# Kernel tuning notes

Measured on AMD Instinct MI355X. Metric: run time of the kernel, lower is better.

The kernel has to match this reference:

```python
import jax, jax.numpy as jnp
import numpy as np

N = 100_000   # nodes
E = 1_600_000 # edges
D = 128       # hidden/input dim
OUT = 32      # output dim
G = 512       # graphs in batch
L = 3         # conv layers


def setup_inputs() -> dict:
    key = jax.random.key(0)
    ks = jax.random.split(key, 12)
    s = 1.0 / np.sqrt(D)
    inp = {
        "x": jax.random.normal(ks[0], (N, D), jnp.float32),
        "edge_index": jax.random.randint(ks[1], (2, E), 0, N, dtype=jnp.int32),
        "batch": jnp.sort(jax.random.randint(ks[2], (N,), 0, G, dtype=jnp.int32)),
        "enc_W1": jax.random.normal(ks[3], (D, D), jnp.float32) * s,
        "enc_b1": jnp.zeros((D,), jnp.float32),
        "enc_W2": jax.random.normal(ks[4], (D, D), jnp.float32) * s,
        "enc_b2": jnp.zeros((D,), jnp.float32),
        "gcn_W": jax.random.normal(ks[5], (L, D, D), jnp.float32) * s,
        "gcn_b": jnp.zeros((L, D), jnp.float32),
        "dec_W1": jax.random.normal(ks[6], (D, D), jnp.float32) * s,
        "dec_b1": jnp.zeros((D,), jnp.float32),
        "dec_W2": jax.random.normal(ks[7], (D, OUT), jnp.float32) * s,
        "dec_b2": jnp.zeros((OUT,), jnp.float32),
        "num_graphs": G,
    }
    return inp


def reference(x, edge_index, batch, enc_W1, enc_b1, enc_W2, enc_b2,
              gcn_W, gcn_b, dec_W1, dec_b1, dec_W2, dec_b2, num_graphs):
    n = x.shape[0]
    src, dst = edge_index[0], edge_index[1]

    # ---- encoder MLP (Linear -> ReLU -> Linear -> ReLU) ----
    h = jax.nn.relu(x @ enc_W1 + enc_b1)
    h = jax.nn.relu(h @ enc_W2 + enc_b2)

    # ---- GCN normalization: D^{-1/2} (A + I) D^{-1/2}, degrees incl. self-loops ----
    deg = jax.ops.segment_sum(jnp.ones_like(src, dtype=h.dtype), dst, num_segments=n) + 1.0
    inv_sqrt = jax.lax.rsqrt(deg)           # [N]
    edge_coef = inv_sqrt[src] * inv_sqrt[dst]  # [E]
    self_coef = inv_sqrt * inv_sqrt            # [N]

    # ---- GCN conv layers ----
    for l in range(gcn_W.shape[0]):
        hw = h @ gcn_W[l]                                       # [N, D]
        msgs = hw[src] * edge_coef[:, None]                     # [E, D] gather
        agg = jax.ops.segment_sum(msgs, dst, num_segments=n)    # [N, D] scatter-add
        agg = agg + hw * self_coef[:, None]                     # self loops
        h = jax.nn.relu(agg + gcn_b[l])

    # ---- global add pool over graphs ----
    pooled = jax.ops.segment_sum(h, batch, num_segments=num_graphs)  # [G, D]

    # ---- decoder MLP ----
    out = jax.nn.relu(pooled @ dec_W1 + dec_b1)
    return out @ dec_W2 + dec_b2
```

## Files before the change

kernel.cpp:

```cpp
#include <hip/hip_runtime.h>

#define NNODES 100000
#define NEDGES 1600000
#define DIM    128
#define OUTD   32
#define NGRAPH 512

#define NBUCK2  256
#define BSHIFT  9
#define CAP     12288
#define EPB2    8192
#define SBLOCKS ((NEDGES + EPB2 - 1) / EPB2)
#define NBUILD  ((NNODES + 511) / 512)
#define EBLOCKS ((NNODES + 63) / 64)
#define AGGBLK  ((NNODES + 31) / 32)

using bf16x8 = __attribute__((ext_vector_type(8))) short;
using f32x4  = __attribute__((ext_vector_type(4))) float;
using f32x2  = __attribute__((ext_vector_type(2))) float;

__device__ __forceinline__ short f2bf(float f) {
    unsigned u = __float_as_uint(f);
    unsigned r = (u + 0x7fff + ((u >> 16) & 1)) >> 16;
    return (short)r;
}
__device__ __forceinline__ float bf2f(short s) {
    return __uint_as_float(((unsigned)(unsigned short)s) << 16);
}

__device__ __forceinline__ uint2 bf8_to_fp8(bf16x8 t) {
    float f0 = bf2f(t[0]), f1 = bf2f(t[1]), f2 = bf2f(t[2]), f3 = bf2f(t[3]);
    float f4 = bf2f(t[4]), f5 = bf2f(t[5]), f6 = bf2f(t[6]), f7 = bf2f(t[7]);
    uint2 o;
    o.x = __builtin_amdgcn_cvt_pk_fp8_f32(f0, f1, 0, false);
    o.x = __builtin_amdgcn_cvt_pk_fp8_f32(f2, f3, o.x, true);
    o.y = __builtin_amdgcn_cvt_pk_fp8_f32(f4, f5, 0, false);
    o.y = __builtin_amdgcn_cvt_pk_fp8_f32(f6, f7, o.y, true);
    return o;
}

__global__ __launch_bounds__(256) void k_prep(
    const float* __restrict__ eW1, const float* __restrict__ eW2,
    const float* __restrict__ gW, short* __restrict__ WT,
    int* __restrict__ gcur, float* __restrict__ pooled)
{
    int idx = blockIdx.x * 256 + threadIdx.x;
    if (idx < 5 * 16384) {
        int mat = idx >> 14, rem = idx & 16383;
        int k = rem >> 7, n = rem & 127;
        const float* src = (mat == 0) ? eW1 : (mat == 1) ? eW2
                                            : (gW + (size_t)(mat - 2) * 16384);
        WT[(size_t)mat * 16384 + n * DIM + k] = f2bf(src[k * DIM + n]);
    }
    if (idx < NBUCK2) gcur[idx] = idx * CAP;
    if (idx < NGRAPH * DIM) pooled[idx] = 0.f;
}

__global__ __launch_bounds__(512) void k_scatter(
    const int* __restrict__ src, const int* __restrict__ dst,
    int* __restrict__ gcur, unsigned* __restrict__ tmp)
{
    __shared__ unsigned short rnk[EPB2];
    __shared__ int h[NBUCK2];
    __shared__ int gbase[NBUCK2];
    const int tid  = threadIdx.x;
    const int base = blockIdx.x * EPB2;
    if (tid < NBUCK2) h[tid] = 0;
    __syncthreads();
    #pragma unroll
    for (int it = 0; it < EPB2 / 512; ++it) {
        int e = base + it * 512 + tid;
        if (e < NEDGES) {
            int b = dst[e] >> BSHIFT;
            rnk[it * 512 + tid] = (unsigned short)atomicAdd(&h[b], 1);
        }
    }
    __syncthreads();
    if (tid < NBUCK2 && h[tid] > 0)
        gbase[tid] = atomicAdd(&gcur[tid], h[tid]);
    __syncthreads();
    #pragma unroll
    for (int it = 0; it < EPB2 / 512; ++it) {
        int e = base + it * 512 + tid;
        if (e < NEDGES) {
            int d = dst[e], sv = src[e];
            int b = d >> BSHIFT;
            int pos = gbase[b] + rnk[it * 512 + tid];
            if (pos < (b + 1) * CAP)
                tmp[pos] = (unsigned)sv | ((unsigned)(d & 511) << 17);
        }
    }
}

__global__ __launch_bounds__(512) void k_build(
    const unsigned* __restrict__ tmp, const int* __restrict__ gcur,
    int* __restrict__ row_off, int* __restrict__ cntA,
    float* __restrict__ inv, int* __restrict__ col)
{
    __shared__ int hist[512], sc[512], lcur[512];
    const int tid   = threadIdx.x;
    const int b     = blockIdx.x;
    const int tbase = b * CAP;
    const int cnt_b = min(gcur[b] - tbase, CAP);
    hist[tid] = 0;
    __syncthreads();
    for (int i = tid; i < cnt_b; i += 512)
        atomicAdd(&hist[(tmp[tbase + i] >> 17) & 511], 1);
    __syncthreads();
    const int hv = hist[tid];
    sc[tid] = hv;
    __syncthreads();
    for (int off = 1; off < 512; off <<= 1) {
        int t = (tid >= off) ? sc[tid - off] : 0;
        __syncthreads();
        sc[tid] += t;
        __syncthreads();
    }
    const int start = tbase + sc[tid] - hv;
    lcur[tid] = start;
    const int node = b * 512 + tid;
    if (node < NNODES) {
        row_off[node] = start;
        cntA[node]    = hv;
        inv[node]     = rsqrtf((float)hv + 1.0f);
    }
    __syncthreads();
    for (int i = tid; i < cnt_b; i += 512) {
        unsigned t = tmp[tbase + i];
        int pos = atomicAdd(&lcur[(t >> 17) & 511], 1);
        col[pos] = (int)((t & 0x1FFFFu) << 7);
    }
}

__global__ __launch_bounds__(512, 6) void k_enc(
    const float* __restrict__ x, const short* __restrict__ WT,
    const float* __restrict__ b1, const float* __restrict__ b2,
    const float* __restrict__ inv, unsigned char* __restrict__ g8, int M)
{
    __shared__ short As[64 * 128];
    __shared__ short Bs[128 * 128];

    const int tid = threadIdx.x;
    const int m0  = blockIdx.x * 64;

    #pragma unroll
    for (int i = 0; i < 2; ++i) {
        int u = tid + i * 512;
        int row = u >> 4, c = u & 15;
        int gr = min(m0 + row, M - 1);
        const float4* sp = (const float4*)(x + (size_t)gr * DIM + (c << 3));
        float4 f0 = sp[0], f1 = sp[1];
        short t8[8] = { f2bf(f0.x), f2bf(f0.y), f2bf(f0.z), f2bf(f0.w),
                        f2bf(f1.x), f2bf(f1.y), f2bf(f1.z), f2bf(f1.w) };
        *(bf16x8*)&As[row * 128 + ((c ^ (row & 15)) << 3)] = *(bf16x8*)t8;
    }

    const int wave = tid >> 6, lane = tid & 63;
    const int ml = lane & 15, quad = lane >> 4;
    const int rw = wave >> 1;
    const int cw = wave & 1;

    #pragma unroll
    for (int mat = 0; mat < 3; ++mat) {
        if (mat > 0) __syncthreads();
        #pragma unroll
        for (int i = 0; i < 4; ++i) {
            int u = tid + i * 512;
            int n = u >> 4, c = u & 15;
            *(bf16x8*)&Bs[n * 128 + ((c ^ (n & 15)) << 3)] =
                *(const bf16x8*)(WT + (size_t)mat * 16384 + n * DIM + (c << 3));
        }
        __syncthreads();

        f32x4 acc[4] = {};
        const int arow = rw * 16 + ml;
        #pragma unroll
        for (int kk = 0; kk < 4; ++kk) {
            const int c = kk * 4 + quad;
            bf16x8 a = *(bf16x8*)&As[arow * 128 + ((c ^ (arow & 15)) << 3)];
            #pragma unroll
            for (int ni = 0; ni < 4; ++ni) {
                const int brow = (cw * 4 + ni) * 16 + ml;
                bf16x8 b = *(bf16x8*)&Bs[brow * 128 + ((c ^ (brow & 15)) << 3)];
                acc[ni] = __builtin_amdgcn_mfma_f32_16x16x32_bf16(a, b, acc[ni], 0, 0, 0);
            }
        }
        __syncthreads();

        #pragma unroll
        for (int ni = 0; ni < 4; ++ni) {
            const int colc = cw * 64 + ni * 16 + ml;
            const int cc = colc >> 3, w = colc & 7;
            #pragma unroll
            for (int r = 0; r < 4; ++r) {
                const int rowl = rw * 16 + quad * 4 + r;
                float v = acc[ni][r];
                if (mat == 0)      v = fmaxf(v + b1[colc], 0.f);
                else if (mat == 1) v = fmaxf(v + b2[colc], 0.f);
                else               v *= inv[min(m0 + rowl, M - 1)];
                As[rowl * 128 + (((cc ^ (rowl & 15)) << 3) | w)] = f2bf(v);
            }
        }
    }
    __syncthreads();

    #pragma unroll
    for (int i = 0; i < 2; ++i) {
        int u = tid + i * 512;
        int row = u >> 4, c = u & 15;
        int gr = m0 + row;
        if (gr < M) {
            bf16x8 t = *(bf16x8*)&As[row * 128 + ((c ^ (row & 15)) << 3)];
            *(uint2*)(g8 + (size_t)gr * DIM + (c << 3)) = bf8_to_fp8(t);
        }
    }
}

#define GATHER_PIPELINE()                                                      \
    const int s = row_off[node];                                               \
    const int e = s + cntA[node];                                              \
    int j = s;                                                                 \
    {                                                                          \
        uint2 b0, b1_, b2_, b3_, b4_, b5_, b6_, b7_;                           \
        const bool hav = (j + 7 < e);                                          \
        if (hav) {                                                             \
            b0 = GLD(col[j]);     b1_ = GLD(col[j + 1]);                       \
            b2_ = GLD(col[j + 2]); b3_ = GLD(col[j + 3]);                      \
            b4_ = GLD(col[j + 4]); b5_ = GLD(col[j + 5]);                      \
            b6_ = GLD(col[j + 6]); b7_ = GLD(col[j + 7]);                      \
            j += 8;                                                            \
        }                                                                      \
        for (; j + 7 < e; j += 8) {                                            \
            uint2 n0 = GLD(col[j]);     uint2 n1 = GLD(col[j + 1]);            \
            uint2 n2 = GLD(col[j + 2]); uint2 n3 = GLD(col[j + 3]);            \
            uint2 n4 = GLD(col[j + 4]); uint2 n5 = GLD(col[j + 5]);            \
            uint2 n6 = GLD(col[j + 6]); uint2 n7 = GLD(col[j + 7]);            \
            ACC8(b0) ACC8(b1_) ACC8(b2_) ACC8(b3_)                             \
            ACC8(b4_) ACC8(b5_) ACC8(b6_) ACC8(b7_)                            \
            b0 = n0; b1_ = n1; b2_ = n2; b3_ = n3;                             \
            b4_ = n4; b5_ = n5; b6_ = n6; b7_ = n7;                            \
        }                                                                      \
        if (hav) {                                                             \
            ACC8(b0) ACC8(b1_) ACC8(b2_) ACC8(b3_)                             \
            ACC8(b4_) ACC8(b5_) ACC8(b6_) ACC8(b7_)                            \
        }                                                                      \
    }                                                                          \
    for (; j + 3 < e; j += 4) {                                                \
        uint2 v0 = GLD(col[j]);     uint2 v1 = GLD(col[j + 1]);                \
        uint2 v2 = GLD(col[j + 2]); uint2 v3 = GLD(col[j + 3]);                \
        ACC8(v0) ACC8(v1) ACC8(v2) ACC8(v3)                                    \
    }                                                                          \
    for (; j < e; ++j) {                                                       \
        uint2 v = GLD(col[j]);                                                 \
        ACC8(v)                                                                \
    }

__global__ __launch_bounds__(512, 8) void k_agg_gemm(
    const unsigned char* __restrict__ g8v, const int* __restrict__ row_off,
    const int* __restrict__ cntA, const int* __restrict__ col,
    const float* __restrict__ inv, const float* __restrict__ bias,
    const short* __restrict__ WT, unsigned char* __restrict__ g8o)
{
    __shared__ short As[32 * 128];
    __shared__ short Bs[128 * 128];

    const int tid = threadIdx.x;

    #pragma unroll
    for (int i = 0; i < 4; ++i) {
        int u = tid + i * 512;
        int n = u >> 4, c = u & 15;
        *(bf16x8*)&Bs[n * 128 + ((c ^ (n & 15)) << 3)] =
            *(const bf16x8*)(WT + n * DIM + (c << 3));
    }

    const int wave = tid >> 6, lane = tid & 63;
    const int q    = lane >> 4;
    const int sl   = lane & 15;
    const int sl8  = sl << 3;
    const int nl   = wave * 4 + q;
    const int m0   = blockIdx.x * 32;
    const int node = m0 + nl;

    f32x2 a01, a23, a45, a67;
    {
        uint2 us = *(const uint2*)(g8v + (size_t)node * 128 + sl8);
        a01 = __builtin_amdgcn_cvt_pk_f32_fp8(us.x, false);
        a23 = __builtin_amdgcn_cvt_pk_f32_fp8(us.x, true);
        a45 = __builtin_amdgcn_cvt_pk_f32_fp8(us.y, false);
        a67 = __builtin_amdgcn_cvt_pk_f32_fp8(us.y, true);
    }

    #define ACC8(v) \
        a01 += __builtin_amdgcn_cvt_pk_f32_fp8(v.x, false); \
        a23 += __builtin_amdgcn_cvt_pk_f32_fp8(v.x, true);  \
        a45 += __builtin_amdgcn_cvt_pk_f32_fp8(v.y, false); \
        a67 += __builtin_amdgcn_cvt_pk_f32_fp8(v.y, true);
    #define GLD(c) (*(const uint2*)(g8v + (size_t)(unsigned)((c) + sl8)))

    GATHER_PIPELINE()

    #undef ACC8
    #undef GLD

    const float scv = inv[node];
    const float4 bb0 = ((const float4*)bias)[sl * 2];
    const float4 bb1 = ((const float4*)bias)[sl * 2 + 1];
    short o[8];
    o[0] = f2bf(fmaxf(fmaf(a01[0], scv, bb0.x), 0.f));
    o[1] = f2bf(fmaxf(fmaf(a01[1], scv, bb0.y), 0.f));
    o[2] = f2bf(fmaxf(fmaf(a23[0], scv, bb0.z), 0.f));
    o[3] = f2bf(fmaxf(fmaf(a23[1], scv, bb0.w), 0.f));
    o[4] = f2bf(fmaxf(fmaf(a45[0], scv, bb1.x), 0.f));
    o[5] = f2bf(fmaxf(fmaf(a45[1], scv, bb1.y), 0.f));
    o[6] = f2bf(fmaxf(fmaf(a67[0], scv, bb1.z), 0.f));
    o[7] = f2bf(fmaxf(fmaf(a67[1], scv, bb1.w), 0.f));
    *(bf16x8*)&As[nl * 128 + ((sl ^ (nl & 15)) << 3)] = *(bf16x8*)o;
    __syncthreads();

    const int mh = wave >> 2;
    const int nq = wave & 3;
    f32x4 acc[2] = {};
    #pragma unroll
    for (int kk = 0; kk < 4; ++kk) {
        const int c = kk * 4 + q;
        bf16x8 a = *(bf16x8*)&As[(mh * 16 + sl) * 128 + ((c ^ sl) << 3)];
        #pragma unroll
        for (int ni = 0; ni < 2; ++ni) {
            bf16x8 b = *(bf16x8*)&Bs[((nq * 2 + ni) * 16 + sl) * 128 + ((c ^ sl) << 3)];
            acc[ni] = __builtin_amdgcn_mfma_f32_16x16x32_bf16(a, b, acc[ni], 0, 0, 0);
        }
    }
    __syncthreads();

    #pragma unroll
    for (int ni = 0; ni < 2; ++ni) {
        const int colc = (nq * 2 + ni) * 16 + sl;
        const int cc   = colc >> 3, cw = colc & 7;
        #pragma unroll
        for (int r = 0; r < 4; ++r) {
            const int rowl = mh * 16 + q * 4 + r;
            As[rowl * 128 + (((cc ^ (rowl & 15)) << 3) | cw)] =
                f2bf(acc[ni][r] * inv[m0 + rowl]);
        }
    }
    __syncthreads();

    {
        int row = tid >> 4, c = tid & 15;
        bf16x8 t = *(bf16x8*)&As[row * 128 + ((c ^ (row & 15)) << 3)];
        *(uint2*)(g8o + (size_t)(m0 + row) * DIM + (c << 3)) = bf8_to_fp8(t);
    }
}

__global__ __launch_bounds__(512) void k_agg_pool(
    const unsigned char* __restrict__ g8v, const int* __restrict__ row_off,
    const int* __restrict__ cntA, const int* __restrict__ col,
    const float* __restrict__ inv, const float* __restrict__ bias,
    const int* __restrict__ batch, float* __restrict__ pooled)
{
    __shared__ float Hs[32][132];
    __shared__ int sbatch[32];

    const int tid = threadIdx.x;
    const int wave = tid >> 6, lane = tid & 63;
    const int q    = lane >> 4;
    const int sl   = lane & 15;
    const int sl8  = sl << 3;
    const int nl   = wave * 4 + q;
    const int m0   = blockIdx.x * 32;
    const int node = m0 + nl;

    if (tid < 32) sbatch[tid] = batch[m0 + tid];

    f32x2 a01, a23, a45, a67;
    {
        uint2 us = *(const uint2*)(g8v + (size_t)node * 128 + sl8);
        a01 = __builtin_amdgcn_cvt_pk_f32_fp8(us.x, false);
        a23 = __builtin_amdgcn_cvt_pk_f32_fp8(us.x, true);
        a45 = __builtin_amdgcn_cvt_pk_f32_fp8(us.y, false);
        a67 = __builtin_amdgcn_cvt_pk_f32_fp8(us.y, true);
    }

    #define ACC8(v) \
        a01 += __builtin_amdgcn_cvt_pk_f32_fp8(v.x, false); \
        a23 += __builtin_amdgcn_cvt_pk_f32_fp8(v.x, true);  \
        a45 += __builtin_amdgcn_cvt_pk_f32_fp8(v.y, false); \
        a67 += __builtin_amdgcn_cvt_pk_f32_fp8(v.y, true);
    #define GLD(c) (*(const uint2*)(g8v + (size_t)(unsigned)((c) + sl8)))

    GATHER_PIPELINE()

    #undef ACC8
    #undef GLD

    const float scv = inv[node];
    const float4 bb0 = ((const float4*)bias)[sl * 2];
    const float4 bb1 = ((const float4*)bias)[sl * 2 + 1];
    float4 h0, h1;
    h0.x = fmaxf(fmaf(a01[0], scv, bb0.x), 0.f);
    h0.y = fmaxf(fmaf(a01[1], scv, bb0.y), 0.f);
    h0.z = fmaxf(fmaf(a23[0], scv, bb0.z), 0.f);
    h0.w = fmaxf(fmaf(a23[1], scv, bb0.w), 0.f);
    h1.x = fmaxf(fmaf(a45[0], scv, bb1.x), 0.f);
    h1.y = fmaxf(fmaf(a45[1], scv, bb1.y), 0.f);
    h1.z = fmaxf(fmaf(a67[0], scv, bb1.z), 0.f);
    h1.w = fmaxf(fmaf(a67[1], scv, bb1.w), 0.f);
    *(float4*)&Hs[nl][sl * 8]     = h0;
    *(float4*)&Hs[nl][sl * 8 + 4] = h1;
    __syncthreads();

    const int d   = tid & 127;
    const int grp = tid >> 7;
    float acc = 0.f;
    int cg = -1;
    #pragma unroll
    for (int i = 0; i < 8; ++i) {
        const int nn = grp * 8 + i;
        const int g  = sbatch[nn];
        if (g != cg) {
            if (cg >= 0) atomicAdd(pooled + (size_t)cg * DIM + d, acc);
            cg = g; acc = 0.f;
        }
        acc += Hs[nn][d];
    }
    atomicAdd(pooled + (size_t)cg * DIM + d, acc);
}

__global__ __launch_bounds__(512) void k_dec(
    const float* __restrict__ pooled, const float* __restrict__ W1,
    const float* __restrict__ b1, const float* __restrict__ W2,
    const float* __restrict__ b2, float* __restrict__ out)
{
    __shared__ float pbuf[8][128];
    __shared__ float tbuf[8][128];
    const int wave = threadIdx.x >> 6, lane = threadIdx.x & 63;
    const int g = blockIdx.x * 8 + wave;

    float2 pv = *(const float2*)(pooled + (size_t)g * DIM + lane * 2);
    pbuf[wave][lane * 2]     = pv.x;
    pbuf[wave][lane * 2 + 1] = pv.y;
    __syncthreads();

    float t0 = 0.f, t1 = 0.f;
    #pragma unroll 8
    for (int k = 0; k < DIM; ++k) {
        float pk = pbuf[wave][k];
        float2 w = *(const float2*)(W1 + (size_t)k * DIM + lane * 2);
        t0 = fmaf(pk, w.x, t0);
        t1 = fmaf(pk, w.y, t1);
    }
    tbuf[wave][lane * 2]     = fmaxf(t0 + b1[lane * 2],     0.f);
    tbuf[wave][lane * 2 + 1] = fmaxf(t1 + b1[lane * 2 + 1], 0.f);
    __syncthreads();

    const int c = lane & 31, hh = lane >> 5;
    float part = 0.f;
    #pragma unroll 8
    for (int kk = 0; kk < 64; ++kk) {
        int k = hh * 64 + kk;
        part = fmaf(tbuf[wave][k], W2[(size_t)k * OUTD + c], part);
    }
    float other = __shfl_xor(part, 32, 64);
    if (hh == 0)
        out[(size_t)g * OUTD + c] = part + other + b2[c];
}

extern "C" void kernel_launch(void* const* d_in, const int* in_sizes, int n_in,
                              void* d_out, int out_size, void* d_ws, size_t ws_size,
                              hipStream_t stream)
{
    const float* x      = (const float*)d_in[0];
    const int*   ei     = (const int*)d_in[1];
    const int*   batch  = (const int*)d_in[2];
    const float* enc_W1 = (const float*)d_in[3];
    const float* enc_b1 = (const float*)d_in[4];
    const float* enc_W2 = (const float*)d_in[5];
    const float* enc_b2 = (const float*)d_in[6];
    const float* gcn_W  = (const float*)d_in[7];
    const float* gcn_b  = (const float*)d_in[8];
    const float* dec_W1 = (const float*)d_in[9];
    const float* dec_b1 = (const float*)d_in[10];
    const float* dec_W2 = (const float*)d_in[11];
    const float* dec_b2 = (const float*)d_in[12];
    float* out = (float*)d_out;

    const int* src = ei;
    const int* dst = ei + NEDGES;

    char* p = (char*)d_ws;
    auto alloc = [&](size_t bytes) -> void* {
        void* r = (void*)p;
        p += (bytes + 255) & ~(size_t)255;
        return r;
    };
    unsigned char* g8a    = (unsigned char*)alloc((size_t)NNODES * DIM);
    unsigned char* g8b    = (unsigned char*)alloc((size_t)NNODES * DIM);
    float*         inv    = (float*)        alloc((size_t)NNODES * sizeof(float));
    int*           row_off= (int*)          alloc((size_t)NNODES * sizeof(int));
    int*           cntA   = (int*)          alloc((size_t)NNODES * sizeof(int));
    int*           col    = (int*)          alloc((size_t)NBUCK2 * CAP * sizeof(int));
    unsigned*      tmp    = (unsigned*)     alloc((size_t)NBUCK2 * CAP * sizeof(unsigned));
    int*           gcur   = (int*)          alloc((size_t)NBUCK2 * sizeof(int));
    short*         WT     = (short*)        alloc((size_t)5 * DIM * DIM * sizeof(short));
    float*         pooled = (float*)        alloc((size_t)NGRAPH * DIM * sizeof(float));

    k_prep   <<<(5 * 16384 + 255) / 256, 256, 0, stream>>>(enc_W1, enc_W2, gcn_W,
                                                           WT, gcur, pooled);
    k_scatter<<<SBLOCKS, 512, 0, stream>>>(src, dst, gcur, tmp);
    k_build  <<<NBUILD, 512, 0, stream>>>(tmp, gcur, row_off, cntA, inv, col);

    k_enc<<<EBLOCKS, 512, 0, stream>>>(x, WT, enc_b1, enc_b2, inv, g8a, NNODES);

    k_agg_gemm<<<AGGBLK, 512, 0, stream>>>(g8a, row_off, cntA, col, inv,
                                           gcn_b,       WT + 3 * 16384, g8b);
    k_agg_gemm<<<AGGBLK, 512, 0, stream>>>(g8b, row_off, cntA, col, inv,
                                           gcn_b + 128, WT + 4 * 16384, g8a);
    k_agg_pool<<<AGGBLK, 512, 0, stream>>>(g8a, row_off, cntA, col, inv,
                                           gcn_b + 256, batch, pooled);

    k_dec <<<NGRAPH / 8, 512, 0, stream>>>(pooled, dec_W1, dec_b1,
                                           dec_W2, dec_b2, out);
}
```

Baseline: 290.9 us.

## Merge prep/scatter and build/encoder kernels, apply source normalization during gather

```diff
diff --git a/kernel.cpp b/kernel.cpp
--- a/kernel.cpp
+++ b/kernel.cpp
@@ -11,9 +11,11 @@
 #define CAP     12288
 #define EPB2    8192
 #define SBLOCKS ((NEDGES + EPB2 - 1) / EPB2)
+#define PREPBLK 160
 #define NBUILD  ((NNODES + 511) / 512)
-#define EBLOCKS ((NNODES + 63) / 64)
+#define EBLK64  ((NNODES + 63) / 64)
 #define AGGBLK  ((NNODES + 31) / 32)
+#define ZBLOCKS ((NBUCK2 + NGRAPH * DIM + 511) / 512)
 
 using bf16x8 = __attribute__((ext_vector_type(8))) short;
 using f32x4  = __attribute__((ext_vector_type(4))) float;
@@ -39,31 +41,33 @@
     return o;
 }
 
-__global__ __launch_bounds__(256) void k_prep(
+__global__ __launch_bounds__(512) void k_zero(int* __restrict__ gz)
+{
+    int idx = blockIdx.x * 512 + threadIdx.x;
+    if (idx < NBUCK2 + NGRAPH * DIM) gz[idx] = 0;
+}
+
+__global__ __launch_bounds__(512) void k_scatter_prep(
+    const int* __restrict__ src, const int* __restrict__ dst,
+    int* __restrict__ gcur, unsigned* __restrict__ tmp,
     const float* __restrict__ eW1, const float* __restrict__ eW2,
-    const float* __restrict__ gW, short* __restrict__ WT,
-    int* __restrict__ gcur, float* __restrict__ pooled)
-{
-    int idx = blockIdx.x * 256 + threadIdx.x;
-    if (idx < 5 * 16384) {
+    const float* __restrict__ gW, short* __restrict__ WT)
+{
+    const int tid = threadIdx.x;
+
+    if (blockIdx.x >= SBLOCKS) {
+        int idx = (blockIdx.x - SBLOCKS) * 512 + tid;
         int mat = idx >> 14, rem = idx & 16383;
         int k = rem >> 7, n = rem & 127;
-        const float* src = (mat == 0) ? eW1 : (mat == 1) ? eW2
-                                            : (gW + (size_t)(mat - 2) * 16384);
-        WT[(size_t)mat * 16384 + n * DIM + k] = f2bf(src[k * DIM + n]);
-    }
-    if (idx < NBUCK2) gcur[idx] = idx * CAP;
-    if (idx < NGRAPH * DIM) pooled[idx] = 0.f;
-}
-
-__global__ __launch_bounds__(512) void k_scatter(
-    const int* __restrict__ src, const int* __restrict__ dst,
-    int* __restrict__ gcur, unsigned* __restrict__ tmp)
-{
+        const float* sp = (mat == 0) ? eW1 : (mat == 1) ? eW2
+                                           : (gW + (size_t)(mat - 2) * 16384);
+        WT[(size_t)mat * 16384 + n * DIM + k] = f2bf(sp[k * DIM + n]);
+        return;
+    }
+
     __shared__ unsigned short rnk[EPB2];
     __shared__ int h[NBUCK2];
     __shared__ int gbase[NBUCK2];
-    const int tid  = threadIdx.x;
     const int base = blockIdx.x * EPB2;
     if (tid < NBUCK2) h[tid] = 0;
     __syncthreads();
@@ -77,7 +81,7 @@
     }
     __syncthreads();
     if (tid < NBUCK2 && h[tid] > 0)
-        gbase[tid] = atomicAdd(&gcur[tid], h[tid]);
+        gbase[tid] = tid * CAP + atomicAdd(&gcur[tid], h[tid]);
     __syncthreads();
     #pragma unroll
     for (int it = 0; it < EPB2 / 512; ++it) {
@@ -92,56 +96,58 @@
     }
 }
 
-__global__ __launch_bounds__(512) void k_build(
+__global__ __launch_bounds__(512, 6) void k_build_enc(
     const unsigned* __restrict__ tmp, const int* __restrict__ gcur,
     int* __restrict__ row_off, int* __restrict__ cntA,
-    float* __restrict__ inv, int* __restrict__ col)
-{
-    __shared__ int hist[512], sc[512], lcur[512];
-    const int tid   = threadIdx.x;
-    const int b     = blockIdx.x;
-    const int tbase = b * CAP;
-    const int cnt_b = min(gcur[b] - tbase, CAP);
-    hist[tid] = 0;
-    __syncthreads();
-    for (int i = tid; i < cnt_b; i += 512)
-        atomicAdd(&hist[(tmp[tbase + i] >> 17) & 511], 1);
-    __syncthreads();
-    const int hv = hist[tid];
-    sc[tid] = hv;
-    __syncthreads();
-    for (int off = 1; off < 512; off <<= 1) {
-        int t = (tid >= off) ? sc[tid - off] : 0;
-        __syncthreads();
-        sc[tid] += t;
-        __syncthreads();
-    }
-    const int start = tbase + sc[tid] - hv;
-    lcur[tid] = start;
-    const int node = b * 512 + tid;
-    if (node < NNODES) {
-        row_off[node] = start;
-        cntA[node]    = hv;
-        inv[node]     = rsqrtf((float)hv + 1.0f);
-    }
-    __syncthreads();
-    for (int i = tid; i < cnt_b; i += 512) {
-        unsigned t = tmp[tbase + i];
-        int pos = atomicAdd(&lcur[(t >> 17) & 511], 1);
-        col[pos] = (int)((t & 0x1FFFFu) << 7);
-    }
-}
-
-__global__ __launch_bounds__(512, 6) void k_enc(
+    float* __restrict__ inv, int* __restrict__ col,
     const float* __restrict__ x, const short* __restrict__ WT,
     const float* __restrict__ b1, const float* __restrict__ b2,
-    const float* __restrict__ inv, unsigned char* __restrict__ g8, int M)
+    unsigned char* __restrict__ g8, int M)
 {
     __shared__ short As[64 * 128];
     __shared__ short Bs[128 * 128];
 
     const int tid = threadIdx.x;
-    const int m0  = blockIdx.x * 64;
+
+    if (blockIdx.x < NBUILD) {
+        int* hist = (int*)As;
+        int* sc   = hist + 512;
+        int* lcur = sc + 512;
+        const int b     = blockIdx.x;
+        const int tbase = b * CAP;
+        const int cnt_b = min(gcur[b], CAP);
+        hist[tid] = 0;
+        __syncthreads();
+        for (int i = tid; i < cnt_b; i += 512)
+            atomicAdd(&hist[(tmp[tbase + i] >> 17) & 511], 1);
+        __syncthreads();
+        const int hv = hist[tid];
+        sc[tid] = hv;
+        __syncthreads();
+        for (int off = 1; off < 512; off <<= 1) {
+            int t = (tid >= off) ? sc[tid - off] : 0;
+            __syncthreads();
+            sc[tid] += t;
+            __syncthreads();
+        }
+        const int start = tbase + sc[tid] - hv;
+        lcur[tid] = start;
+        const int node = b * 512 + tid;
+        if (node < NNODES) {
+            row_off[node] = start;
+            cntA[node]    = hv;
+            inv[node]     = rsqrtf((float)hv + 1.0f);
+        }
+        __syncthreads();
+        for (int i = tid; i < cnt_b; i += 512) {
+            unsigned t = tmp[tbase + i];
+            int pos = atomicAdd(&lcur[(t >> 17) & 511], 1);
+            col[pos] = (int)((t & 0x1FFFFu) << 7);
+        }
+        return;
+    }
+
+    const int m0 = (blockIdx.x - NBUILD) * 64;
 
     #pragma unroll
     for (int i = 0; i < 2; ++i) {
@@ -197,7 +203,6 @@
                 float v = acc[ni][r];
                 if (mat == 0)      v = fmaxf(v + b1[colc], 0.f);
                 else if (mat == 1) v = fmaxf(v + b2[colc], 0.f);
-                else               v *= inv[min(m0 + rowl, M - 1)];
                 As[rowl * 128 + (((cc ^ (rowl & 15)) << 3) | w)] = f2bf(v);
             }
         }
@@ -216,43 +221,57 @@
     }
 }
 
+#define ACCS(v, s_) { \
+    f32x2 sv_ = {s_, s_}; \
+    a01 += __builtin_amdgcn_cvt_pk_f32_fp8(v.x, false) * sv_; \
+    a23 += __builtin_amdgcn_cvt_pk_f32_fp8(v.x, true)  * sv_; \
+    a45 += __builtin_amdgcn_cvt_pk_f32_fp8(v.y, false) * sv_; \
+    a67 += __builtin_amdgcn_cvt_pk_f32_fp8(v.y, true)  * sv_; }
+
 #define GATHER_PIPELINE()                                                      \
-    const int s = row_off[node];                                               \
-    const int e = s + cntA[node];                                              \
-    int j = s;                                                                 \
+    const int rs = row_off[node];                                              \
+    const int re = rs + cntA[node];                                            \
+    int j = rs;                                                                \
     {                                                                          \
-        uint2 b0, b1_, b2_, b3_, b4_, b5_, b6_, b7_;                           \
-        const bool hav = (j + 7 < e);                                          \
+        uint2 r0, r1, r2, r3, r4, r5, r6, r7;                                  \
+        float s0, s1, s2, s3, s4, s5, s6, s7;                                  \
+        const bool hav = (j + 7 < re);                                         \
         if (hav) {                                                             \
-            b0 = GLD(col[j]);     b1_ = GLD(col[j + 1]);                       \
-            b2_ = GLD(col[j + 2]); b3_ = GLD(col[j + 3]);                      \
-            b4_ = GLD(col[j + 4]); b5_ = GLD(col[j + 5]);                      \
-            b6_ = GLD(col[j + 6]); b7_ = GLD(col[j + 7]);                      \
+            int c0=col[j],c1=col[j+1],c2=col[j+2],c3=col[j+3];                 \
+            int c4=col[j+4],c5=col[j+5],c6=col[j+6],c7=col[j+7];               \
+            r0=GLD(c0); r1=GLD(c1); r2=GLD(c2); r3=GLD(c3);                    \
+            r4=GLD(c4); r5=GLD(c5); r6=GLD(c6); r7=GLD(c7);                    \
+            s0=SLD(c0); s1=SLD(c1); s2=SLD(c2); s3=SLD(c3);                    \
+            s4=SLD(c4); s5=SLD(c5); s6=SLD(c6); s7=SLD(c7);                    \
             j += 8;                                                            \
         }                                                                      \
-        for (; j + 7 < e; j += 8) {                                            \
-            uint2 n0 = GLD(col[j]);     uint2 n1 = GLD(col[j + 1]);            \
-            uint2 n2 = GLD(col[j + 2]); uint2 n3 = GLD(col[j + 3]);            \
-            uint2 n4 = GLD(col[j + 4]); uint2 n5 = GLD(col[j + 5]);            \
-            uint2 n6 = GLD(col[j + 6]); uint2 n7 = GLD(col[j + 7]);            \
-            ACC8(b0) ACC8(b1_) ACC8(b2_) ACC8(b3_)                             \
-            ACC8(b4_) ACC8(b5_) ACC8(b6_) ACC8(b7_)                            \
-            b0 = n0; b1_ = n1; b2_ = n2; b3_ = n3;                             \
-            b4_ = n4; b5_ = n5; b6_ = n6; b7_ = n7;                            \
+        for (; j + 7 < re; j += 8) {                                           \
+            int c0=col[j],c1=col[j+1],c2=col[j+2],c3=col[j+3];                 \
+            int c4=col[j+4],c5=col[j+5],c6=col[j+6],c7=col[j+7];               \
+            uint2 n0=GLD(c0),n1=GLD(c1),n2=GLD(c2),n3=GLD(c3);                 \
+            uint2 n4=GLD(c4),n5=GLD(c5),n6=GLD(c6),n7=GLD(c7);                 \
+            float t0=SLD(c0),t1=SLD(c1),t2=SLD(c2),t3=SLD(c3);                 \
+            float t4=SLD(c4),t5=SLD(c5),t6=SLD(c6),t7=SLD(c7);                 \
+            ACCS(r0,s0) ACCS(r1,s1) ACCS(r2,s2) ACCS(r3,s3)                    \
+            ACCS(r4,s4) ACCS(r5,s5) ACCS(r6,s6) ACCS(r7,s7)                    \
+            r0=n0; r1=n1; r2=n2; r3=n3; r4=n4; r5=n5; r6=n6; r7=n7;            \
+            s0=t0; s1=t1; s2=t2; s3=t3; s4=t4; s5=t5; s6=t6; s7=t7;            \
         }                                                                      \
         if (hav) {                                                             \
-            ACC8(b0) ACC8(b1_) ACC8(b2_) ACC8(b3_)                             \
-            ACC8(b4_) ACC8(b5_) ACC8(b6_) ACC8(b7_)                            \
+            ACCS(r0,s0) ACCS(r1,s1) ACCS(r2,s2) ACCS(r3,s3)                    \
+            ACCS(r4,s4) ACCS(r5,s5) ACCS(r6,s6) ACCS(r7,s7)                    \
         }                                                                      \
     }                                                                          \
-    for (; j + 3 < e; j += 4) {                                                \
-        uint2 v0 = GLD(col[j]);     uint2 v1 = GLD(col[j + 1]);                \
-        uint2 v2 = GLD(col[j + 2]); uint2 v3 = GLD(col[j + 3]);                \
-        ACC8(v0) ACC8(v1) ACC8(v2) ACC8(v3)                                    \
+    for (; j + 3 < re; j += 4) {                                               \
+        int c0=col[j],c1=col[j+1],c2=col[j+2],c3=col[j+3];                     \
+        uint2 v0=GLD(c0),v1=GLD(c1),v2=GLD(c2),v3=GLD(c3);                     \
+        float u0=SLD(c0),u1=SLD(c1),u2=SLD(c2),u3=SLD(c3);                     \
+        ACCS(v0,u0) ACCS(v1,u1) ACCS(v2,u2) ACCS(v3,u3)                        \
     }                                                                          \
-    for (; j < e; ++j) {                                                       \
-        uint2 v = GLD(col[j]);                                                 \
-        ACC8(v)                                                                \
+    for (; j < re; ++j) {                                                      \
+        int c0 = col[j];                                                       \
+        uint2 v = GLD(c0); float u0 = SLD(c0);                                 \
+        ACCS(v, u0)                                                            \
     }
 
 __global__ __launch_bounds__(512, 8) void k_agg_gemm(
@@ -282,28 +301,25 @@
     const int m0   = blockIdx.x * 32;
     const int node = m0 + nl;
 
+    #define GLD(c) (*(const uint2*)(g8v + (size_t)(unsigned)((c) + sl8)))
+    #define SLD(c) (inv[(unsigned)(c) >> 7])
+
+    const float scv = inv[node];
     f32x2 a01, a23, a45, a67;
     {
         uint2 us = *(const uint2*)(g8v + (size_t)node * 128 + sl8);
-        a01 = __builtin_amdgcn_cvt_pk_f32_fp8(us.x, false);
-        a23 = __builtin_amdgcn_cvt_pk_f32_fp8(us.x, true);
-        a45 = __builtin_amdgcn_cvt_pk_f32_fp8(us.y, false);
-        a67 = __builtin_amdgcn_cvt_pk_f32_fp8(us.y, true);
-    }
-
-    #define ACC8(v) \
-        a01 += __builtin_amdgcn_cvt_pk_f32_fp8(v.x, false); \
-        a23 += __builtin_amdgcn_cvt_pk_f32_fp8(v.x, true);  \
-        a45 += __builtin_amdgcn_cvt_pk_f32_fp8(v.y, false); \
-        a67 += __builtin_amdgcn_cvt_pk_f32_fp8(v.y, true);
-    #define GLD(c) (*(const uint2*)(g8v + (size_t)(unsigned)((c) + sl8)))
+        f32x2 sv2 = {scv, scv};
+        a01 = __builtin_amdgcn_cvt_pk_f32_fp8(us.x, false) * sv2;
+        a23 = __builtin_amdgcn_cvt_pk_f32_fp8(us.x, true)  * sv2;
+        a45 = __builtin_amdgcn_cvt_pk_f32_fp8(us.y, false) * sv2;
+        a67 = __builtin_amdgcn_cvt_pk_f32_fp8(us.y, true)  * sv2;
+    }
 
     GATHER_PIPELINE()
 
-    #undef ACC8
     #undef GLD
-
-    const float scv = inv[node];
+    #undef SLD
+
     const float4 bb0 = ((const float4*)bias)[sl * 2];
     const float4 bb1 = ((const float4*)bias)[sl * 2 + 1];
     short o[8];
@@ -341,7 +357,7 @@
         for (int r = 0; r < 4; ++r) {
             const int rowl = mh * 16 + q * 4 + r;
             As[rowl * 128 + (((cc ^ (rowl & 15)) << 3) | cw)] =
-                f2bf(acc[ni][r] * inv[m0 + rowl]);
+                f2bf(acc[ni][r]);
         }
     }
     __syncthreads();
@@ -373,28 +389,25 @@
 
     if (tid < 32) sbatch[tid] = batch[m0 + tid];
 
+    #define GLD(c) (*(const uint2*)(g8v + (size_t)(unsigned)((c) + sl8)))
+    #define SLD(c) (inv[(unsigned)(c) >> 7])
+
+    const float scv = inv[node];
     f32x2 a01, a23, a45, a67;
     {
         uint2 us = *(const uint2*)(g8v + (size_t)node * 128 + sl8);
-        a01 = __builtin_amdgcn_cvt_pk_f32_fp8(us.x, false);
-        a23 = __builtin_amdgcn_cvt_pk_f32_fp8(us.x, true);
-        a45 = __builtin_amdgcn_cvt_pk_f32_fp8(us.y, false);
-        a67 = __builtin_amdgcn_cvt_pk_f32_fp8(us.y, true);
-    }
-
-    #define ACC8(v) \
-        a01 += __builtin_amdgcn_cvt_pk_f32_fp8(v.x, false); \
-        a23 += __builtin_amdgcn_cvt_pk_f32_fp8(v.x, true);  \
-        a45 += __builtin_amdgcn_cvt_pk_f32_fp8(v.y, false); \
-        a67 += __builtin_amdgcn_cvt_pk_f32_fp8(v.y, true);
-    #define GLD(c) (*(const uint2*)(g8v + (size_t)(unsigned)((c) + sl8)))
+        f32x2 sv2 = {scv, scv};
+        a01 = __builtin_amdgcn_cvt_pk_f32_fp8(us.x, false) * sv2;
+        a23 = __builtin_amdgcn_cvt_pk_f32_fp8(us.x, true)  * sv2;
+        a45 = __builtin_amdgcn_cvt_pk_f32_fp8(us.y, false) * sv2;
+        a67 = __builtin_amdgcn_cvt_pk_f32_fp8(us.y, true)  * sv2;
+    }
 
     GATHER_PIPELINE()
 
-    #undef ACC8
     #undef GLD
-
-    const float scv = inv[node];
+    #undef SLD
+
     const float4 bb0 = ((const float4*)bias)[sl * 2];
     const float4 bb1 = ((const float4*)bias)[sl * 2 + 1];
     float4 h0, h1;
@@ -494,6 +507,8 @@
         p += (bytes + 255) & ~(size_t)255;
         return r;
     };
+    int*           gcur   = (int*)          alloc((size_t)NBUCK2 * sizeof(int));
+    float*         pooled = (float*)        alloc((size_t)NGRAPH * DIM * sizeof(float));
     unsigned char* g8a    = (unsigned char*)alloc((size_t)NNODES * DIM);
     unsigned char* g8b    = (unsigned char*)alloc((size_t)NNODES * DIM);
     float*         inv    = (float*)        alloc((size_t)NNODES * sizeof(float));
@@ -501,16 +516,16 @@
     int*           cntA   = (int*)          alloc((size_t)NNODES * sizeof(int));
     int*           col    = (int*)          alloc((size_t)NBUCK2 * CAP * sizeof(int));
     unsigned*      tmp    = (unsigned*)     alloc((size_t)NBUCK2 * CAP * sizeof(unsigned));
-    int*           gcur   = (int*)          alloc((size_t)NBUCK2 * sizeof(int));
     short*         WT     = (short*)        alloc((size_t)5 * DIM * DIM * sizeof(short));
-    float*         pooled = (float*)        alloc((size_t)NGRAPH * DIM * sizeof(float));
-
-    k_prep   <<<(5 * 16384 + 255) / 256, 256, 0, stream>>>(enc_W1, enc_W2, gcn_W,
-                                                           WT, gcur, pooled);
-    k_scatter<<<SBLOCKS, 512, 0, stream>>>(src, dst, gcur, tmp);
-    k_build  <<<NBUILD, 512, 0, stream>>>(tmp, gcur, row_off, cntA, inv, col);
-
-    k_enc<<<EBLOCKS, 512, 0, stream>>>(x, WT, enc_b1, enc_b2, inv, g8a, NNODES);
+
+    k_zero<<<ZBLOCKS, 512, 0, stream>>>(gcur);
+
+    k_scatter_prep<<<SBLOCKS + PREPBLK, 512, 0, stream>>>(
+        src, dst, gcur, tmp, enc_W1, enc_W2, gcn_W, WT);
+
+    k_build_enc<<<NBUILD + EBLK64, 512, 0, stream>>>(
+        tmp, gcur, row_off, cntA, inv, col,
+        x, WT, enc_b1, enc_b2, g8a, NNODES);
 
     k_agg_gemm<<<AGGBLK, 512, 0, stream>>>(g8a, row_off, cntA, col, inv,
                                            gcn_b,       WT + 3 * 16384, g8b);
```

After: 299.2 us. +2.9%, slower.

## Merge preprocessing kernels and compute degrees via global atomics to overlap build with encoder

Applied to the files above, without the earlier changes.

```diff
diff --git a/kernel.cpp b/kernel.cpp
--- a/kernel.cpp
+++ b/kernel.cpp
@@ -11,9 +11,12 @@
 #define CAP     12288
 #define EPB2    8192
 #define SBLOCKS ((NEDGES + EPB2 - 1) / EPB2)
+#define PREPBLK 160
 #define NBUILD  ((NNODES + 511) / 512)
-#define EBLOCKS ((NNODES + 63) / 64)
+#define EBLK64  ((NNODES + 63) / 64)
 #define AGGBLK  ((NNODES + 31) / 32)
+#define NZERO   (NBUCK2 + NGRAPH * DIM + NNODES)
+#define ZBLOCKS ((NZERO + 511) / 512)
 
 using bf16x8 = __attribute__((ext_vector_type(8))) short;
 using f32x4  = __attribute__((ext_vector_type(4))) float;
@@ -39,31 +42,34 @@
     return o;
 }
 
-__global__ __launch_bounds__(256) void k_prep(
+__global__ __launch_bounds__(512) void k_zero(int* __restrict__ gz)
+{
+    int idx = blockIdx.x * 512 + threadIdx.x;
+    if (idx < NZERO) gz[idx] = 0;
+}
+
+__global__ __launch_bounds__(512) void k_scatter_prep(
+    const int* __restrict__ src, const int* __restrict__ dst,
+    int* __restrict__ gcur, unsigned* __restrict__ tmp,
+    int* __restrict__ deg,
     const float* __restrict__ eW1, const float* __restrict__ eW2,
-    const float* __restrict__ gW, short* __restrict__ WT,
-    int* __restrict__ gcur, float* __restrict__ pooled)
-{
-    int idx = blockIdx.x * 256 + threadIdx.x;
-    if (idx < 5 * 16384) {
+    const float* __restrict__ gW, short* __restrict__ WT)
+{
+    const int tid = threadIdx.x;
+
+    if (blockIdx.x >= SBLOCKS) {
+        int idx = (blockIdx.x - SBLOCKS) * 512 + tid;
         int mat = idx >> 14, rem = idx & 16383;
         int k = rem >> 7, n = rem & 127;
-        const float* src = (mat == 0) ? eW1 : (mat == 1) ? eW2
-                                            : (gW + (size_t)(mat - 2) * 16384);
-        WT[(size_t)mat * 16384 + n * DIM + k] = f2bf(src[k * DIM + n]);
-    }
-    if (idx < NBUCK2) gcur[idx] = idx * CAP;
-    if (idx < NGRAPH * DIM) pooled[idx] = 0.f;
-}
-
-__global__ __launch_bounds__(512) void k_scatter(
-    const int* __restrict__ src, const int* __restrict__ dst,
-    int* __restrict__ gcur, unsigned* __restrict__ tmp)
-{
+        const float* sp = (mat == 0) ? eW1 : (mat == 1) ? eW2
+                                           : (gW + (size_t)(mat - 2) * 16384);
+        WT[(size_t)mat * 16384 + n * DIM + k] = f2bf(sp[k * DIM + n]);
+        return;
+    }
+
     __shared__ unsigned short rnk[EPB2];
     __shared__ int h[NBUCK2];
     __shared__ int gbase[NBUCK2];
-    const int tid  = threadIdx.x;
     const int base = blockIdx.x * EPB2;
     if (tid < NBUCK2) h[tid] = 0;
     __syncthreads();
@@ -71,13 +77,14 @@
     for (int it = 0; it < EPB2 / 512; ++it) {
         int e = base + it * 512 + tid;
         if (e < NEDGES) {
-            int b = dst[e] >> BSHIFT;
-            rnk[it * 512 + tid] = (unsigned short)atomicAdd(&h[b], 1);
+            int d = dst[e];
+            rnk[it * 512 + tid] = (unsigned short)atomicAdd(&h[d >> BSHIFT], 1);
+            atomicAdd(&deg[d], 1);
         }
     }
     __syncthreads();
     if (tid < NBUCK2 && h[tid] > 0)
-        gbase[tid] = atomicAdd(&gcur[tid], h[tid]);
+        gbase[tid] = tid * CAP + atomicAdd(&gcur[tid], h[tid]);
     __syncthreads();
     #pragma unroll
     for (int it = 0; it < EPB2 / 512; ++it) {
@@ -92,56 +99,59 @@
     }
 }
 
-__global__ __launch_bounds__(512) void k_build(
+__global__ __launch_bounds__(512, 6) void k_build_enc(
     const unsigned* __restrict__ tmp, const int* __restrict__ gcur,
     int* __restrict__ row_off, int* __restrict__ cntA,
-    float* __restrict__ inv, int* __restrict__ col)
-{
-    __shared__ int hist[512], sc[512], lcur[512];
-    const int tid   = threadIdx.x;
-    const int b     = blockIdx.x;
-    const int tbase = b * CAP;
-    const int cnt_b = min(gcur[b] - tbase, CAP);
-    hist[tid] = 0;
-    __syncthreads();
-    for (int i = tid; i < cnt_b; i += 512)
-        atomicAdd(&hist[(tmp[tbase + i] >> 17) & 511], 1);
-    __syncthreads();
-    const int hv = hist[tid];
-    sc[tid] = hv;
-    __syncthreads();
-    for (int off = 1; off < 512; off <<= 1) {
-        int t = (tid >= off) ? sc[tid - off] : 0;
-        __syncthreads();
-        sc[tid] += t;
-        __syncthreads();
-    }
-    const int start = tbase + sc[tid] - hv;
-    lcur[tid] = start;
-    const int node = b * 512 + tid;
-    if (node < NNODES) {
-        row_off[node] = start;
-        cntA[node]    = hv;
-        inv[node]     = rsqrtf((float)hv + 1.0f);
-    }
-    __syncthreads();
-    for (int i = tid; i < cnt_b; i += 512) {
-        unsigned t = tmp[tbase + i];
-        int pos = atomicAdd(&lcur[(t >> 17) & 511], 1);
-        col[pos] = (int)((t & 0x1FFFFu) << 7);
-    }
-}
-
-__global__ __launch_bounds__(512, 6) void k_enc(
+    float* __restrict__ inv, int* __restrict__ col,
+    const int* __restrict__ deg,
     const float* __restrict__ x, const short* __restrict__ WT,
     const float* __restrict__ b1, const float* __restrict__ b2,
-    const float* __restrict__ inv, unsigned char* __restrict__ g8, int M)
+    unsigned char* __restrict__ g8, int M)
 {
     __shared__ short As[64 * 128];
     __shared__ short Bs[128 * 128];
 
     const int tid = threadIdx.x;
-    const int m0  = blockIdx.x * 64;
+
+    if (blockIdx.x < NBUILD) {
+        int* hist = (int*)As;
+        int* sc   = hist + 512;
+        int* lcur = sc + 512;
+        const int b     = blockIdx.x;
+        const int tbase = b * CAP;
+        const int cnt_b = min(gcur[b], CAP);
+        hist[tid] = 0;
+        __syncthreads();
+        for (int i = tid; i < cnt_b; i += 512)
+            atomicAdd(&hist[(tmp[tbase + i] >> 17) & 511], 1);
+        __syncthreads();
+        const int hv = hist[tid];
+        sc[tid] = hv;
+        __syncthreads();
+        for (int off = 1; off < 512; off <<= 1) {
+            int t = (tid >= off) ? sc[tid - off] : 0;
+            __syncthreads();
+            sc[tid] += t;
+            __syncthreads();
+        }
+        const int start = tbase + sc[tid] - hv;
+        lcur[tid] = start;
+        const int node = b * 512 + tid;
+        if (node < NNODES) {
+            row_off[node] = start;
+            cntA[node]    = hv;
+            inv[node]     = rsqrtf((float)hv + 1.0f);
+        }
+        __syncthreads();
+        for (int i = tid; i < cnt_b; i += 512) {
+            unsigned t = tmp[tbase + i];
+            int pos = atomicAdd(&lcur[(t >> 17) & 511], 1);
+            col[pos] = (int)((t & 0x1FFFFu) << 7);
+        }
+        return;
+    }
+
+    const int m0 = (blockIdx.x - NBUILD) * 64;
 
     #pragma unroll
     for (int i = 0; i < 2; ++i) {
@@ -197,7 +207,8 @@
                 float v = acc[ni][r];
                 if (mat == 0)      v = fmaxf(v + b1[colc], 0.f);
                 else if (mat == 1) v = fmaxf(v + b2[colc], 0.f);
-                else               v *= inv[min(m0 + rowl, M - 1)];
+                else
+                    v *= rsqrtf((float)deg[min(m0 + rowl, M - 1)] + 1.0f);
                 As[rowl * 128 + (((cc ^ (rowl & 15)) << 3) | w)] = f2bf(v);
             }
         }
@@ -217,12 +228,12 @@
 }
 
 #define GATHER_PIPELINE()                                                      \
-    const int s = row_off[node];                                               \
-    const int e = s + cntA[node];                                              \
-    int j = s;                                                                 \
+    const int rs = row_off[node];                                              \
+    const int re = rs + cntA[node];                                            \
+    int j = rs;                                                                \
     {                                                                          \
         uint2 b0, b1_, b2_, b3_, b4_, b5_, b6_, b7_;                           \
-        const bool hav = (j + 7 < e);                                          \
+        const bool hav = (j + 7 < re);                                         \
         if (hav) {                                                             \
             b0 = GLD(col[j]);     b1_ = GLD(col[j + 1]);                       \
             b2_ = GLD(col[j + 2]); b3_ = GLD(col[j + 3]);                      \
@@ -230,7 +241,7 @@
             b6_ = GLD(col[j + 6]); b7_ = GLD(col[j + 7]);                      \
             j += 8;                                                            \
         }                                                                      \
-        for (; j + 7 < e; j += 8) {                                            \
+        for (; j + 7 < re; j += 8) {                                           \
             uint2 n0 = GLD(col[j]);     uint2 n1 = GLD(col[j + 1]);            \
             uint2 n2 = GLD(col[j + 2]); uint2 n3 = GLD(col[j + 3]);            \
             uint2 n4 = GLD(col[j + 4]); uint2 n5 = GLD(col[j + 5]);            \
@@ -245,12 +256,12 @@
             ACC8(b4_) ACC8(b5_) ACC8(b6_) ACC8(b7_)                            \
         }                                                                      \
     }                                                                          \
-    for (; j + 3 < e; j += 4) {                                                \
+    for (; j + 3 < re; j += 4) {                                               \
         uint2 v0 = GLD(col[j]);     uint2 v1 = GLD(col[j + 1]);                \
         uint2 v2 = GLD(col[j + 2]); uint2 v3 = GLD(col[j + 3]);                \
         ACC8(v0) ACC8(v1) ACC8(v2) ACC8(v3)                                    \
     }                                                                          \
-    for (; j < e; ++j) {                                                       \
+    for (; j < re; ++j) {                                                      \
         uint2 v = GLD(col[j]);                                                 \
         ACC8(v)                                                                \
     }
@@ -494,6 +505,9 @@
         p += (bytes + 255) & ~(size_t)255;
         return r;
     };
+    int*           gcur   = (int*)          alloc((size_t)NBUCK2 * sizeof(int));
+    float*         pooled = (float*)        alloc((size_t)NGRAPH * DIM * sizeof(float));
+    int*           deg    = (int*)          alloc((size_t)NNODES * sizeof(int));
     unsigned char* g8a    = (unsigned char*)alloc((size_t)NNODES * DIM);
     unsigned char* g8b    = (unsigned char*)alloc((size_t)NNODES * DIM);
     float*         inv    = (float*)        alloc((size_t)NNODES * sizeof(float));
@@ -501,16 +515,16 @@
     int*           cntA   = (int*)          alloc((size_t)NNODES * sizeof(int));
     int*           col    = (int*)          alloc((size_t)NBUCK2 * CAP * sizeof(int));
     unsigned*      tmp    = (unsigned*)     alloc((size_t)NBUCK2 * CAP * sizeof(unsigned));
-    int*           gcur   = (int*)          alloc((size_t)NBUCK2 * sizeof(int));
     short*         WT     = (short*)        alloc((size_t)5 * DIM * DIM * sizeof(short));
-    float*         pooled = (float*)        alloc((size_t)NGRAPH * DIM * sizeof(float));
-
-    k_prep   <<<(5 * 16384 + 255) / 256, 256, 0, stream>>>(enc_W1, enc_W2, gcn_W,
-                                                           WT, gcur, pooled);
-    k_scatter<<<SBLOCKS, 512, 0, stream>>>(src, dst, gcur, tmp);
-    k_build  <<<NBUILD, 512, 0, stream>>>(tmp, gcur, row_off, cntA, inv, col);
-
-    k_enc<<<EBLOCKS, 512, 0, stream>>>(x, WT, enc_b1, enc_b2, inv, g8a, NNODES);
+
+    k_zero<<<ZBLOCKS, 512, 0, stream>>>(gcur);
+
+    k_scatter_prep<<<SBLOCKS + PREPBLK, 512, 0, stream>>>(
+        src, dst, gcur, tmp, deg, enc_W1, enc_W2, gcn_W, WT);
+
+    k_build_enc<<<NBUILD + EBLK64, 512, 0, stream>>>(
+        tmp, gcur, row_off, cntA, inv, col, deg,
+        x, WT, enc_b1, enc_b2, g8a, NNODES);
 
     k_agg_gemm<<<AGGBLK, 512, 0, stream>>>(g8a, row_off, cntA, col, inv,
                                            gcn_b,       WT + 3 * 16384, g8b);
```

Measured after the change: 340.1 us. 16.9% more time.
